# Kernel optimization log

Hardware: AMD Instinct MI355X
Metric: run time of the kernel (lower is better)

Reference implementation:

```python
import jax, jax.numpy as jnp
import numpy as np

HID = 64
HEADS = 4
HEAD_DIM = HID // HEADS
N_MOL, N_PROT = 2048, 4096
E_MOL, E_PROT = 32768, 131072
B = 32


def _lin(key, din, dout):
    kw, kb = jax.random.split(key)
    s = 1.0 / np.sqrt(din)
    W = jax.random.uniform(kw, (din, dout), jnp.float32, -s, s)
    b = jax.random.uniform(kb, (dout,), jnp.float32, -s, s)
    return W, b


def setup_inputs() -> dict:
    key = jax.random.key(0)
    ks = jax.random.split(key, 32)
    inp = {}
    inp['mol_x'] = jax.random.normal(ks[0], (N_MOL, 11), jnp.float32)
    inp['prot_x'] = jax.random.normal(ks[1], (N_PROT, 15), jnp.float32)
    inp['mol_eattr'] = jax.random.normal(ks[2], (E_MOL, 10), jnp.float32)
    inp['prot_eattr'] = jax.random.normal(ks[3], (E_PROT, 10), jnp.float32)
    inp['mol_edge_index'] = jax.random.randint(ks[4], (2, E_MOL), 0, N_MOL, jnp.int32)
    inp['prot_edge_index'] = jax.random.randint(ks[5], (2, E_PROT), 0, N_PROT, jnp.int32)
    inp['mol_batch'] = jnp.sort(jax.random.randint(ks[6], (N_MOL,), 0, B, jnp.int32))
    inp['prot_batch'] = jnp.sort(jax.random.randint(ks[7], (N_PROT,), 0, B, jnp.int32))
    inp['node_lin_mol_W'], inp['node_lin_mol_b'] = _lin(ks[8], 11, HID)
    inp['node_lin_prot_W'], inp['node_lin_prot_b'] = _lin(ks[9], 15, HID)
    inp['edge_lin_mol_W'], inp['edge_lin_mol_b'] = _lin(ks[10], 10, HID)
    inp['edge_lin_prot_W'], inp['edge_lin_prot_b'] = _lin(ks[11], 10, HID)
    for pref, base in (('mol_conv', 12), ('prot_conv', 15)):
        W1s, b1s, W2s, b2s = [], [], [], []
        for l in range(3):
            k1, k2 = jax.random.split(ks[base + l])
            W1, b1 = _lin(k1, HID, HID)
            W2, b2 = _lin(k2, HID, HID)
            W1s.append(W1); b1s.append(b1); W2s.append(W2); b2s.append(b2)
        inp[pref + '_W1'] = jnp.stack(W1s); inp[pref + '_b1'] = jnp.stack(b1s)
        inp[pref + '_W2'] = jnp.stack(W2s); inp[pref + '_b2'] = jnp.stack(b2s)
    for pref, base in (('attn_mp', 18), ('attn_pm', 21)):
        Ws, bs = [], []
        for i in range(3):  # Q, K, V
            W, b = _lin(ks[base + i], HID, HID)
            Ws.append(W); bs.append(b)
        inp[pref + '_W'] = jnp.stack(Ws); inp[pref + '_b'] = jnp.stack(bs)
    inp['fc1_W'], inp['fc1_b'] = _lin(ks[24], 2 * HID, HID)
    inp['fc2_W'], inp['fc2_b'] = _lin(ks[25], HID, 1)
    return inp


def _gine_layer(x, src, dst, eattr, W1, b1, W2, b2):
    # message: ReLU(x_j + e_ji); GINEConv sum aggregation; eps = 0
    msg = jax.nn.relu(x[src] + eattr)                       # [E, H]
    agg = jax.ops.segment_sum(msg, dst, num_segments=x.shape[0])
    h = x + agg
    h = jax.nn.relu(h @ W1 + b1) @ W2 + b2                  # inner MLP
    return jax.nn.relu(h)                                   # post-conv ReLU


def _cross_attn(qn, kn, W, b):
    Nq, Nk = qn.shape[0], kn.shape[0]
    Q = (qn @ W[0] + b[0]).reshape(Nq, HEADS, HEAD_DIM)
    K = (kn @ W[1] + b[1]).reshape(Nk, HEADS, HEAD_DIM)
    V = (kn @ W[2] + b[2]).reshape(Nk, HEADS, HEAD_DIM)
    scores = jnp.einsum('qhd,khd->hqk', Q, K) / np.sqrt(HEAD_DIM)
    w = jax.nn.softmax(scores, axis=-1)
    out = jnp.einsum('hqk,khd->qhd', w, V)
    return out.reshape(Nq, HID)


def _pool(H, batch):
    s = jax.ops.segment_sum(H, batch, num_segments=B)
    c = jax.ops.segment_sum(jnp.ones((H.shape[0],), H.dtype), batch, num_segments=B)
    return s / jnp.maximum(c, 1.0)[:, None]


def _forward(mol_x, prot_x, mol_eattr, prot_eattr,
             node_lin_mol_W, node_lin_mol_b, node_lin_prot_W, node_lin_prot_b,
             edge_lin_mol_W, edge_lin_mol_b, edge_lin_prot_W, edge_lin_prot_b,
             mol_conv_W1, mol_conv_b1, mol_conv_W2, mol_conv_b2,
             prot_conv_W1, prot_conv_b1, prot_conv_W2, prot_conv_b2,
             attn_mp_W, attn_mp_b, attn_pm_W, attn_pm_b,
             fc1_W, fc1_b, fc2_W, fc2_b,
             mol_edge_index, prot_edge_index, mol_batch, prot_batch):
    xm = mol_x @ node_lin_mol_W + node_lin_mol_b
    xp = prot_x @ node_lin_prot_W + node_lin_prot_b
    em = mol_eattr @ edge_lin_mol_W + edge_lin_mol_b
    ep = prot_eattr @ edge_lin_prot_W + edge_lin_prot_b
    ms, md = mol_edge_index[0], mol_edge_index[1]
    ps, pd = prot_edge_index[0], prot_edge_index[1]
    for l in range(3):
        xm = _gine_layer(xm, ms, md, em, mol_conv_W1[l], mol_conv_b1[l], mol_conv_W2[l], mol_conv_b2[l])
    for l in range(3):
        xp = _gine_layer(xp, ps, pd, ep, prot_conv_W1[l], prot_conv_b1[l], prot_conv_W2[l], prot_conv_b2[l])
    H_mol = xm + _cross_attn(xm, xp, attn_mp_W, attn_mp_b)
    H_prot = xp + _cross_attn(xp, xm, attn_pm_W, attn_pm_b)
    z = jnp.concatenate([_pool(H_mol, mol_batch), _pool(H_prot, prot_batch)], axis=1)
    h = jax.nn.relu(z @ fc1_W + fc1_b)
    return jax.nn.sigmoid(h @ fc2_W + fc2_b).squeeze(-1)


def reference(mol_x, prot_x, mol_eattr, prot_eattr,
              node_lin_mol_W, node_lin_mol_b, node_lin_prot_W, node_lin_prot_b,
              edge_lin_mol_W, edge_lin_mol_b, edge_lin_prot_W, edge_lin_prot_b,
              mol_conv_W1, mol_conv_b1, mol_conv_W2, mol_conv_b2,
              prot_conv_W1, prot_conv_b1, prot_conv_W2, prot_conv_b2,
              attn_mp_W, attn_mp_b, attn_pm_W, attn_pm_b,
              fc1_W, fc1_b, fc2_W, fc2_b,
              mol_edge_index, prot_edge_index, mol_batch, prot_batch):
    return _forward(mol_x, prot_x, mol_eattr, prot_eattr,
                    node_lin_mol_W, node_lin_mol_b, node_lin_prot_W, node_lin_prot_b,
                    edge_lin_mol_W, edge_lin_mol_b, edge_lin_prot_W, edge_lin_prot_b,
                    mol_conv_W1, mol_conv_b1, mol_conv_W2, mol_conv_b2,
                    prot_conv_W1, prot_conv_b1, prot_conv_W2, prot_conv_b2,
                    attn_mp_W, attn_mp_b, attn_pm_W, attn_pm_b,
                    fc1_W, fc1_b, fc2_W, fc2_b,
                    mol_edge_index, prot_edge_index, mol_batch, prot_batch)
```

## Files before the change

### kernel.cpp

```cpp
#include <hip/hip_runtime.h>
#include <math.h>

#define HID 64
#define HEADS 4
#define HDIM 16
#define N_MOL 2048
#define N_PROT 4096
#define E_MOL 32768
#define E_PROT 131072
#define BATCH 32
#define N_TOT (N_MOL + N_PROT)
#define E_TOT (E_MOL + E_PROT)
#define CAP 128

#define TQA 16
#define TKA 32
#define KSTA 68
#define CH_MOL 8
#define CH_PROT 2
#define NGRP_MOL (N_MOL / TQA)

#define DOT4(a, b) ((a).x*(b).x + (a).y*(b).y + (a).z*(b).z + (a).w*(b).w)
#define EXP2(x) __builtin_amdgcn_exp2f(x)

__global__ void k_nlb(const float* __restrict__ mol_x, const float* __restrict__ prot_x,
                      const float* __restrict__ Wm, const float* __restrict__ bm,
                      const float* __restrict__ Wp, const float* __restrict__ bp,
                      const int* __restrict__ mol_ei, const int* __restrict__ prot_ei,
                      float* __restrict__ xm, float* __restrict__ xp,
                      int* __restrict__ cursor, int* __restrict__ eidx) {
    if (blockIdx.x < N_TOT / 4) {
        int w = threadIdx.x >> 6, t = threadIdx.x & 63;
        int n = blockIdx.x * 4 + w;
        if (n < N_MOL) {
            const float* xr = mol_x + n * 11;
            float acc = bm[t];
#pragma unroll
            for (int i = 0; i < 11; ++i) acc += xr[i] * Wm[i * HID + t];
            xm[n * HID + t] = acc;
        } else {
            int p = n - N_MOL;
            const float* xr = prot_x + p * 15;
            float acc = bp[t];
#pragma unroll
            for (int i = 0; i < 15; ++i) acc += xr[i] * Wp[i * HID + t];
            xp[p * HID + t] = acc;
        }
    } else {
        int e = (blockIdx.x - N_TOT / 4) * 256 + threadIdx.x;
        int node, loc;
        if (e < E_MOL) { node = mol_ei[E_MOL + e]; loc = e; }
        else { int el = e - E_MOL; node = N_MOL + prot_ei[E_PROT + el]; loc = el; }
        int pos = atomicAdd(&cursor[node], 1);
        eidx[(size_t)node * CAP + pos] = loc;
    }
}

__global__ void k_gine(const float* __restrict__ xin_m, const float* __restrict__ xin_p,
                       float* __restrict__ xout_m, float* __restrict__ xout_p,
                       const float* __restrict__ mol_ea, const float* __restrict__ prot_ea,
                       const int* __restrict__ mol_ei, const int* __restrict__ prot_ei,
                       const float* __restrict__ Wem, const float* __restrict__ bem,
                       const float* __restrict__ Wep, const float* __restrict__ bep,
                       const float* __restrict__ W1m, const float* __restrict__ b1m,
                       const float* __restrict__ W2m, const float* __restrict__ b2m,
                       const float* __restrict__ W1p, const float* __restrict__ b1p,
                       const float* __restrict__ W2p, const float* __restrict__ b2p,
                       const int* __restrict__ cnt, const int* __restrict__ eidx) {
    __shared__ float h0[8][HID];
    __shared__ float h1[8][HID];
    int w = threadIdx.x >> 6, t = threadIdx.x & 63;
    int nb0 = blockIdx.x * 8 + w * 2;
    bool isMol = nb0 < N_MOL;
    const float* x  = isMol ? xin_m : xin_p;
    float* xo       = isMol ? xout_m : xout_p;
    const float* We = isMol ? Wem : Wep;
    float bt        = isMol ? bem[t] : bep[t];
    const float* ea_base = isMol ? mol_ea : prot_ea;
    const int* srcarr    = isMol ? mol_ei : prot_ei;
    int nbias = isMol ? 0 : N_MOL;
    float wcol[10];
#pragma unroll
    for (int i = 0; i < 10; ++i) wcol[i] = We[i * HID + t];

#pragma unroll
    for (int u = 0; u < 2; ++u) {
        int nb = nb0 + u;
        int deg = cnt[nb];
        const int* lst = eidx + (size_t)nb * CAP;
        float agg = 0.f;
        int j = 0;
        for (; j + 1 < deg; j += 2) {
            int e0 = lst[j], e1 = lst[j + 1];
            int s0 = srcarr[e0], s1 = srcarr[e1];
            const float2* p0 = (const float2*)(ea_base + (size_t)e0 * 10);
            const float2* p1 = (const float2*)(ea_base + (size_t)e1 * 10);
            float2 a0 = p0[0], a1 = p0[1], a2 = p0[2], a3 = p0[3], a4 = p0[4];
            float2 c0 = p1[0], c1 = p1[1], c2 = p1[2], c3 = p1[3], c4 = p1[4];
            float xs0 = x[s0 * HID + t];
            float xs1 = x[s1 * HID + t];
            float m0 = bt, m1 = bt;
            m0 = fmaf(a0.x, wcol[0], m0); m0 = fmaf(a0.y, wcol[1], m0);
            m0 = fmaf(a1.x, wcol[2], m0); m0 = fmaf(a1.y, wcol[3], m0);
            m0 = fmaf(a2.x, wcol[4], m0); m0 = fmaf(a2.y, wcol[5], m0);
            m0 = fmaf(a3.x, wcol[6], m0); m0 = fmaf(a3.y, wcol[7], m0);
            m0 = fmaf(a4.x, wcol[8], m0); m0 = fmaf(a4.y, wcol[9], m0);
            m1 = fmaf(c0.x, wcol[0], m1); m1 = fmaf(c0.y, wcol[1], m1);
            m1 = fmaf(c1.x, wcol[2], m1); m1 = fmaf(c1.y, wcol[3], m1);
            m1 = fmaf(c2.x, wcol[4], m1); m1 = fmaf(c2.y, wcol[5], m1);
            m1 = fmaf(c3.x, wcol[6], m1); m1 = fmaf(c3.y, wcol[7], m1);
            m1 = fmaf(c4.x, wcol[8], m1); m1 = fmaf(c4.y, wcol[9], m1);
            agg += fmaxf(m0 + xs0, 0.f) + fmaxf(m1 + xs1, 0.f);
        }
        if (j < deg) {
            int e0 = lst[j];
            int s0 = srcarr[e0];
            const float2* p0 = (const float2*)(ea_base + (size_t)e0 * 10);
            float2 a0 = p0[0], a1 = p0[1], a2 = p0[2], a3 = p0[3], a4 = p0[4];
            float xs0 = x[s0 * HID + t];
            float m0 = bt;
            m0 = fmaf(a0.x, wcol[0], m0); m0 = fmaf(a0.y, wcol[1], m0);
            m0 = fmaf(a1.x, wcol[2], m0); m0 = fmaf(a1.y, wcol[3], m0);
            m0 = fmaf(a2.x, wcol[4], m0); m0 = fmaf(a2.y, wcol[5], m0);
            m0 = fmaf(a3.x, wcol[6], m0); m0 = fmaf(a3.y, wcol[7], m0);
            m0 = fmaf(a4.x, wcol[8], m0); m0 = fmaf(a4.y, wcol[9], m0);
            agg += fmaxf(m0 + xs0, 0.f);
        }
        h0[w * 2 + u][t] = x[(nb0 - nbias + u) * HID + t] + agg;
    }

    const float* W1 = isMol ? W1m : W1p;
    const float* W2 = isMol ? W2m : W2p;
    float b1v = isMol ? b1m[t] : b1p[t];
    float b2v = isMol ? b2m[t] : b2p[t];
    float acc0 = b1v, acc1 = b1v;
    const float4* hA = (const float4*)h0[w * 2];
    const float4* hB = (const float4*)h0[w * 2 + 1];
#pragma unroll
    for (int k = 0; k < 16; ++k) {
        float4 a = hA[k], b = hB[k];
        float w0 = W1[(4 * k + 0) * HID + t], w1 = W1[(4 * k + 1) * HID + t];
        float w2 = W1[(4 * k + 2) * HID + t], w3 = W1[(4 * k + 3) * HID + t];
        acc0 = fmaf(a.x, w0, acc0); acc1 = fmaf(b.x, w0, acc1);
        acc0 = fmaf(a.y, w1, acc0); acc1 = fmaf(b.y, w1, acc1);
        acc0 = fmaf(a.z, w2, acc0); acc1 = fmaf(b.z, w2, acc1);
        acc0 = fmaf(a.w, w3, acc0); acc1 = fmaf(b.w, w3, acc1);
    }
    h1[w * 2][t] = fmaxf(acc0, 0.f);
    h1[w * 2 + 1][t] = fmaxf(acc1, 0.f);
    float d0 = b2v, d1 = b2v;
    const float4* gA = (const float4*)h1[w * 2];
    const float4* gB = (const float4*)h1[w * 2 + 1];
#pragma unroll
    for (int k = 0; k < 16; ++k) {
        float4 a = gA[k], b = gB[k];
        float w0 = W2[(4 * k + 0) * HID + t], w1 = W2[(4 * k + 1) * HID + t];
        float w2 = W2[(4 * k + 2) * HID + t], w3 = W2[(4 * k + 3) * HID + t];
        d0 = fmaf(a.x, w0, d0); d1 = fmaf(b.x, w0, d1);
        d0 = fmaf(a.y, w1, d0); d1 = fmaf(b.y, w1, d1);
        d0 = fmaf(a.z, w2, d0); d1 = fmaf(b.z, w2, d1);
        d0 = fmaf(a.w, w3, d0); d1 = fmaf(b.w, w3, d1);
    }
    int n0 = nb0 - nbias;
    xo[n0 * HID + t] = fmaxf(d0, 0.f);
    xo[(n0 + 1) * HID + t] = fmaxf(d1, 0.f);
}

__global__ void k_qkv(const float* __restrict__ xm, const float* __restrict__ xp,
                      const float* __restrict__ mpW, const float* __restrict__ mpb,
                      const float* __restrict__ pmW, const float* __restrict__ pmb,
                      float* __restrict__ Qm, float* __restrict__ Kp, float* __restrict__ Vp,
                      float* __restrict__ Qp, float* __restrict__ Km, float* __restrict__ Vm) {
    __shared__ float row[8][HID];
    int w = threadIdx.x >> 6, t = threadIdx.x & 63;
    int b0 = blockIdx.x * 8;
    const float *src, *W, *bias;
    float* dst;
    int base;
    if (b0 < 2048)       { base = 0;     src = xm; W = mpW;        bias = mpb;       dst = Qm; }
    else if (b0 < 6144)  { base = 2048;  src = xp; W = mpW + 4096; bias = mpb + 64;  dst = Kp; }
    else if (b0 < 10240) { base = 6144;  src = xp; W = mpW + 8192; bias = mpb + 128; dst = Vp; }
    else if (b0 < 14336) { base = 10240; src = xp; W = pmW;        bias = pmb;       dst = Qp; }
    else if (b0 < 16384) { base = 14336; src = xm; W = pmW + 4096; bias = pmb + 64;  dst = Km; }
    else                 { base = 16384; src = xm; W = pmW + 8192; bias = pmb + 128; dst = Vm; }
    int n0 = b0 - base + w * 2, n1 = n0 + 1;
    row[w * 2][t] = src[n0 * HID + t];
    row[w * 2 + 1][t] = src[n1 * HID + t];
    float acc0 = bias[t], acc1 = acc0;
    const float4* rA = (const float4*)row[w * 2];
    const float4* rB = (const float4*)row[w * 2 + 1];
#pragma unroll
    for (int k = 0; k < 16; ++k) {
        float4 a = rA[k], b = rB[k];
        float w0 = W[(4 * k + 0) * HID + t], w1 = W[(4 * k + 1) * HID + t];
        float w2 = W[(4 * k + 2) * HID + t], w3 = W[(4 * k + 3) * HID + t];
        acc0 = fmaf(a.x, w0, acc0); acc1 = fmaf(b.x, w0, acc1);
        acc0 = fmaf(a.y, w1, acc0); acc1 = fmaf(b.y, w1, acc1);
        acc0 = fmaf(a.z, w2, acc0); acc1 = fmaf(b.z, w2, acc1);
        acc0 = fmaf(a.w, w3, acc0); acc1 = fmaf(b.w, w3, acc1);
    }
    dst[n0 * HID + t] = acc0;
    dst[n1 * HID + t] = acc1;
}

__device__ inline void upd4(float4& A, const float4 v0, const float4 v1,
                            float p0, float p1, float al) {
    A.x = fmaf(p1, v1.x, fmaf(p0, v0.x, A.x * al));
    A.y = fmaf(p1, v1.y, fmaf(p0, v0.y, A.y * al));
    A.z = fmaf(p1, v1.z, fmaf(p0, v0.z, A.z * al));
    A.w = fmaf(p1, v1.w, fmaf(p0, v0.w, A.w * al));
}

__device__ inline void merge4(float4& A, const float4 B, float c1, float c2) {
    A.x = A.x * c1 + B.x * c2;
    A.y = A.y * c1 + B.y * c2;
    A.z = A.z * c1 + B.z * c2;
    A.w = A.w * c1 + B.w * c2;
}

__device__ inline float4 shfl4(const float4 a, int off) {
    float4 r;
    r.x = __shfl_xor(a.x, off, 64); r.y = __shfl_xor(a.y, off, 64);
    r.z = __shfl_xor(a.z, off, 64); r.w = __shfl_xor(a.w, off, 64);
    return r;
}

__global__ __launch_bounds__(256) void k_attn(
    const float* __restrict__ Qm, const float* __restrict__ Kp, const float* __restrict__ Vp,
    const float* __restrict__ Qp, const float* __restrict__ Km, const float* __restrict__ Vm,
    float* __restrict__ part_m, float* __restrict__ part_p) {
    __shared__ float Kl[2][TKA * KSTA];
    __shared__ float Vl[2][TKA * KSTA];

    int t = threadIdx.x;
    const float *Q, *K, *V;
    float* part;
    int q0, chunk, CH, KC;
    {
        int b = blockIdx.x;
        const int MOLB = NGRP_MOL * CH_MOL;
        if (b < MOLB) {
            chunk = b & 7; q0 = (b >> 3) * TQA; CH = CH_MOL; KC = N_PROT / CH_MOL;
            Q = Qm; K = Kp; V = Vp; part = part_m;
        } else {
            b -= MOLB;
            chunk = b & 1; q0 = (b >> 1) * TQA; CH = CH_PROT; KC = N_MOL / CH_PROT;
            Q = Qp; K = Km; V = Vm; part = part_p;
        }
    }
    int kbeg = chunk * KC;

    int sub = t & 15, h = (t >> 4) & 3, qg = t >> 6;
    int r0 = t >> 4;
    int c0 = (t & 15) << 2;

    const float sc = 0.25f * 1.44269504088896f;
    float4 q4[4][4];
#pragma unroll
    for (int qq = 0; qq < 4; ++qq) {
        const float4* Qr = (const float4*)(Q + (q0 + qg * 4 + qq) * HID + h * HDIM);
#pragma unroll
        for (int j = 0; j < 4; ++j) {
            float4 v = Qr[j];
            v.x *= sc; v.y *= sc; v.z *= sc; v.w *= sc;
            q4[qq][j] = v;
        }
    }

    float mreg[4], lreg[4];
    float4 A[4][4];
#pragma unroll
    for (int qq = 0; qq < 4; ++qq) {
        mreg[qq] = -INFINITY; lreg[qq] = 0.f;
#pragma unroll
        for (int j = 0; j < 4; ++j) A[qq][j] = (float4){0.f, 0.f, 0.f, 0.f};
    }

    {
        const float4* Kg = (const float4*)(K + kbeg * HID);
        const float4* Vg = (const float4*)(V + kbeg * HID);
        float4 ka = Kg[t], kb = Kg[t + 256];
        float4 va = Vg[t], vb = Vg[t + 256];
        *(float4*)&Kl[0][r0 * KSTA + c0] = ka;
        *(float4*)&Kl[0][(r0 + 16) * KSTA + c0] = kb;
        *(float4*)&Vl[0][r0 * KSTA + c0] = va;
        *(float4*)&Vl[0][(r0 + 16) * KSTA + c0] = vb;
    }
    __syncthreads();

    const int NT = KC / TKA;
    for (int tile = 0; tile < NT; ++tile) {
        int cur = tile & 1;
        float4 ka, kb, va, vb;
        bool more = (tile + 1) < NT;
        if (more) {
            const float4* Kg = (const float4*)(K + (kbeg + (tile + 1) * TKA) * HID);
            const float4* Vg = (const float4*)(V + (kbeg + (tile + 1) * TKA) * HID);
            ka = Kg[t]; kb = Kg[t + 256];
            va = Vg[t]; vb = Vg[t + 256];
        }

        const float4* Kr0 = (const float4*)&Kl[cur][sub * KSTA + h * HDIM];
        const float4* Kr1 = (const float4*)&Kl[cur][(sub + 16) * KSTA + h * HDIM];
        float4 x0 = Kr0[0], x1 = Kr0[1], x2 = Kr0[2], x3 = Kr0[3];
        float4 y0 = Kr1[0], y1 = Kr1[1], y2 = Kr1[2], y3 = Kr1[3];

        float s0[4], s1[4];
#pragma unroll
        for (int qq = 0; qq < 4; ++qq) {
            s0[qq] = DOT4(x0, q4[qq][0]) + DOT4(x1, q4[qq][1]) + DOT4(x2, q4[qq][2]) + DOT4(x3, q4[qq][3]);
            s1[qq] = DOT4(y0, q4[qq][0]) + DOT4(y1, q4[qq][1]) + DOT4(y2, q4[qq][2]) + DOT4(y3, q4[qq][3]);
        }

        const float4* Vr0 = (const float4*)&Vl[cur][sub * KSTA + h * HDIM];
        const float4* Vr1 = (const float4*)&Vl[cur][(sub + 16) * KSTA + h * HDIM];
        float4 v00 = Vr0[0], v01 = Vr0[1], v02 = Vr0[2], v03 = Vr0[3];
        float4 v10 = Vr1[0], v11 = Vr1[1], v12 = Vr1[2], v13 = Vr1[3];

#pragma unroll
        for (int qq = 0; qq < 4; ++qq) {
            float mn = fmaxf(mreg[qq], fmaxf(s0[qq], s1[qq]));
            float al = EXP2(mreg[qq] - mn);
            float p0 = EXP2(s0[qq] - mn);
            float p1 = EXP2(s1[qq] - mn);
            lreg[qq] = lreg[qq] * al + p0 + p1;
            upd4(A[qq][0], v00, v10, p0, p1, al);
            upd4(A[qq][1], v01, v11, p0, p1, al);
            upd4(A[qq][2], v02, v12, p0, p1, al);
            upd4(A[qq][3], v03, v13, p0, p1, al);
            mreg[qq] = mn;
        }

        if (more) {
            int nxt = cur ^ 1;
            *(float4*)&Kl[nxt][r0 * KSTA + c0] = ka;
            *(float4*)&Kl[nxt][(r0 + 16) * KSTA + c0] = kb;
            *(float4*)&Vl[nxt][r0 * KSTA + c0] = va;
            *(float4*)&Vl[nxt][(r0 + 16) * KSTA + c0] = vb;
        }
        __syncthreads();
    }

#pragma unroll
    for (int off = 1; off < 16; off <<= 1) {
#pragma unroll
        for (int qq = 0; qq < 4; ++qq) {
            float m2 = __shfl_xor(mreg[qq], off, 64);
            float l2 = __shfl_xor(lreg[qq], off, 64);
            float4 B0 = shfl4(A[qq][0], off), B1 = shfl4(A[qq][1], off);
            float4 B2 = shfl4(A[qq][2], off), B3 = shfl4(A[qq][3], off);
            float mn = fmaxf(mreg[qq], m2);
            float c1 = EXP2(mreg[qq] - mn), c2 = EXP2(m2 - mn);
            lreg[qq] = lreg[qq] * c1 + l2 * c2;
            merge4(A[qq][0], B0, c1, c2); merge4(A[qq][1], B1, c1, c2);
            merge4(A[qq][2], B2, c1, c2); merge4(A[qq][3], B3, c1, c2);
            mreg[qq] = mn;
        }
    }

    if (sub == 0) {
#pragma unroll
        for (int qq = 0; qq < 4; ++qq) {
            int qi = q0 + qg * 4 + qq;
            float* pp = part + (size_t)((qi * HEADS + h) * CH + chunk) * 20;
            pp[0] = mreg[qq]; pp[1] = lreg[qq];
            *(float4*)&pp[4] = A[qq][0]; *(float4*)&pp[8] = A[qq][1];
            *(float4*)&pp[12] = A[qq][2]; *(float4*)&pp[16] = A[qq][3];
        }
    }
}

__global__ void k_final(const float* __restrict__ part_m, const float* __restrict__ part_p,
                        const float* __restrict__ xm, const float* __restrict__ xp,
                        const int* __restrict__ mb, const int* __restrict__ pb,
                        const float* __restrict__ fc1W, const float* __restrict__ fc1b,
                        const float* __restrict__ fc2W, const float* __restrict__ fc2b,
                        float* __restrict__ out) {
    __shared__ float sm[64][65];
    __shared__ float z[2 * HID];
    int b = blockIdx.x;
    int t = threadIdx.x;
    int h = t & 3, s = t >> 2;
    int ms, me, ps, pe;
    {
        int lo = 0, hi = N_MOL;
        while (lo < hi) { int mid = (lo + hi) >> 1; if (mb[mid] < b) lo = mid + 1; else hi = mid; }
        ms = lo; lo = ms; hi = N_MOL;
        while (lo < hi) { int mid = (lo + hi) >> 1; if (mb[mid] < b + 1) lo = mid + 1; else hi = mid; }
        me = lo;
        lo = 0; hi = N_PROT;
        while (lo < hi) { int mid = (lo + hi) >> 1; if (pb[mid] < b) lo = mid + 1; else hi = mid; }
        ps = lo; lo = ps; hi = N_PROT;
        while (lo < hi) { int mid = (lo + hi) >> 1; if (pb[mid] < b + 1) lo = mid + 1; else hi = mid; }
        pe = lo;
    }

    {
        float acc[16];
#pragma unroll
        for (int d = 0; d < 16; ++d) acc[d] = 0.f;
        for (int q = ms + s; q < me; q += 64) {
            const float* p0 = part_m + (size_t)(q * HEADS + h) * CH_MOL * 20;
            float mmax = -INFINITY;
#pragma unroll
            for (int c = 0; c < CH_MOL; ++c) mmax = fmaxf(mmax, p0[c * 20]);
            float lsum = 0.f, wgt[CH_MOL];
#pragma unroll
            for (int c = 0; c < CH_MOL; ++c) {
                wgt[c] = EXP2(p0[c * 20] - mmax);
                lsum += p0[c * 20 + 1] * wgt[c];
            }
            float inv = 1.f / lsum;
            const float* Xr = xm + q * HID + h * HDIM;
#pragma unroll
            for (int d = 0; d < 16; ++d) {
                float o = Xr[d];
#pragma unroll
                for (int c = 0; c < CH_MOL; ++c)
                    o = fmaf(p0[c * 20 + 4 + d], wgt[c] * inv, o);
                acc[d] += o;
            }
        }
#pragma unroll
        for (int d = 0; d < 16; ++d) sm[s][h * 16 + d] = acc[d];
    }
    __syncthreads();
    if (t < 64) {
        float sum = 0.f;
        for (int ss = 0; ss < 64; ++ss) sum += sm[ss][t];
        z[t] = sum / fmaxf((float)(me - ms), 1.f);
    }
    __syncthreads();

    {
        float acc[16];
#pragma unroll
        for (int d = 0; d < 16; ++d) acc[d] = 0.f;
        for (int q = ps + s; q < pe; q += 64) {
            const float* p0 = part_p + (size_t)(q * HEADS + h) * CH_PROT * 20;
            float m0 = p0[0], m1 = p0[20];
            float mmax = fmaxf(m0, m1);
            float w0 = EXP2(m0 - mmax), w1 = EXP2(m1 - mmax);
            float inv = 1.f / (p0[1] * w0 + p0[21] * w1);
            w0 *= inv; w1 *= inv;
            const float* Xr = xp + q * HID + h * HDIM;
#pragma unroll
            for (int d = 0; d < 16; ++d)
                acc[d] += Xr[d] + p0[4 + d] * w0 + p0[24 + d] * w1;
        }
#pragma unroll
        for (int d = 0; d < 16; ++d) sm[s][h * 16 + d] = acc[d];
    }
    __syncthreads();
    if (t < 64) {
        float sum = 0.f;
        for (int ss = 0; ss < 64; ++ss) sum += sm[ss][t];
        z[64 + t] = sum / fmaxf((float)(pe - ps), 1.f);
    }
    __syncthreads();

    if (t < 64) {
        float acc = fc1b[t];
        const float4* zv = (const float4*)z;
#pragma unroll
        for (int k = 0; k < 32; ++k) {
            float4 hv = zv[k];
            acc = fmaf(hv.x, fc1W[(4 * k + 0) * 64 + t], acc);
            acc = fmaf(hv.y, fc1W[(4 * k + 1) * 64 + t], acc);
            acc = fmaf(hv.z, fc1W[(4 * k + 2) * 64 + t], acc);
            acc = fmaf(hv.w, fc1W[(4 * k + 3) * 64 + t], acc);
        }
        float hv = fmaxf(acc, 0.f);
        float prod = hv * fc2W[t];
#pragma unroll
        for (int off = 32; off > 0; off >>= 1) prod += __shfl_xor(prod, off, 64);
        if (t == 0) out[b] = 1.f / (1.f + __expf(-(prod + fc2b[0])));
    }
}

extern "C" void kernel_launch(void* const* d_in, const int* in_sizes, int n_in,
                              void* d_out, int out_size, void* d_ws, size_t ws_size,
                              hipStream_t stream) {
    const float* mol_x   = (const float*)d_in[0];
    const float* prot_x  = (const float*)d_in[1];
    const float* mol_ea  = (const float*)d_in[2];
    const float* prot_ea = (const float*)d_in[3];
    const int*   mol_ei  = (const int*)d_in[4];
    const int*   prot_ei = (const int*)d_in[5];
    const int*   mol_b   = (const int*)d_in[6];
    const int*   prot_b  = (const int*)d_in[7];
    const float* nlmW = (const float*)d_in[8];
    const float* nlmb = (const float*)d_in[9];
    const float* nlpW = (const float*)d_in[10];
    const float* nlpb = (const float*)d_in[11];
    const float* elmW = (const float*)d_in[12];
    const float* elmb = (const float*)d_in[13];
    const float* elpW = (const float*)d_in[14];
    const float* elpb = (const float*)d_in[15];
    const float* mcW1 = (const float*)d_in[16];
    const float* mcb1 = (const float*)d_in[17];
    const float* mcW2 = (const float*)d_in[18];
    const float* mcb2 = (const float*)d_in[19];
    const float* pcW1 = (const float*)d_in[20];
    const float* pcb1 = (const float*)d_in[21];
    const float* pcW2 = (const float*)d_in[22];
    const float* pcb2 = (const float*)d_in[23];
    const float* mpW  = (const float*)d_in[24];
    const float* mpb  = (const float*)d_in[25];
    const float* pmW  = (const float*)d_in[26];
    const float* pmb  = (const float*)d_in[27];
    const float* fc1W = (const float*)d_in[28];
    const float* fc1b = (const float*)d_in[29];
    const float* fc2W = (const float*)d_in[30];
    const float* fc2b = (const float*)d_in[31];

    float* ws    = (float*)d_ws;
    float* xa_m  = ws;
    float* xa_p  = xa_m + 131072;
    float* xb_m  = xa_p + 262144;
    float* xb_p  = xb_m + 131072;
    float* Qm    = xb_p + 262144;
    float* Kp    = Qm + 131072;
    float* Vp    = Kp + 262144;
    float* Qp    = Vp + 262144;
    float* Km    = Qp + 262144;
    float* Vm    = Km + 131072;
    float* partm = Vm + 131072;
    float* partp = partm + 1310720;
    int* cursor  = (int*)(partp + 655360);
    int* eidx    = (int*)partm;

    hipMemsetAsync(cursor, 0, (size_t)N_TOT * 4, stream);

    k_nlb<<<N_TOT / 4 + E_TOT / 256, 256, 0, stream>>>(
        mol_x, prot_x, nlmW, nlmb, nlpW, nlpb, mol_ei, prot_ei, xa_m, xa_p, cursor, eidx);

    k_gine<<<N_TOT / 8, 256, 0, stream>>>(xa_m, xa_p, xb_m, xb_p, mol_ea, prot_ea, mol_ei, prot_ei,
        elmW, elmb, elpW, elpb,
        mcW1, mcb1, mcW2, mcb2, pcW1, pcb1, pcW2, pcb2, cursor, eidx);
    k_gine<<<N_TOT / 8, 256, 0, stream>>>(xb_m, xb_p, xa_m, xa_p, mol_ea, prot_ea, mol_ei, prot_ei,
        elmW, elmb, elpW, elpb,
        mcW1 + 4096, mcb1 + 64, mcW2 + 4096, mcb2 + 64,
        pcW1 + 4096, pcb1 + 64, pcW2 + 4096, pcb2 + 64, cursor, eidx);
    k_gine<<<N_TOT / 8, 256, 0, stream>>>(xa_m, xa_p, xb_m, xb_p, mol_ea, prot_ea, mol_ei, prot_ei,
        elmW, elmb, elpW, elpb,
        mcW1 + 8192, mcb1 + 128, mcW2 + 8192, mcb2 + 128,
        pcW1 + 8192, pcb1 + 128, pcW2 + 8192, pcb2 + 128, cursor, eidx);

    k_qkv<<<18432 / 8, 256, 0, stream>>>(xb_m, xb_p, mpW, mpb, pmW, pmb, Qm, Kp, Vp, Qp, Km, Vm);
    k_attn<<<NGRP_MOL * CH_MOL + (N_PROT / TQA) * CH_PROT, 256, 0, stream>>>(
        Qm, Kp, Vp, Qp, Km, Vm, partm, partp);

    k_final<<<BATCH, 256, 0, stream>>>(partm, partp, xb_m, xb_p, mol_b, prot_b,
                                       fc1W, fc1b, fc2W, fc2b, (float*)d_out);
}
```

Before: 385.4 us.

## Fuse all stages into one cooperative persistent kernel with grid syncs

Replaces the memset and seven separate kernel launches with a single cooperative kernel. Blocks loop over virtual block indices for each stage: edge bucketing, the three GINE layers, QKV, attention and the final pooling, with grid-wide syncs in between. The mol attention key split drops from 8 to 4 chunks so fewer partials need storing and merging. This removes launch gaps and inter-kernel drain, but it caps the grid at 1024 blocks, adds grid barrier costs, and the union shared memory sized for attention may limit occupancy.

After: 1.406 ms. +264.9%, slower.

```diff
diff --git a/kernel.cpp b/kernel.cpp
--- a/kernel.cpp
+++ b/kernel.cpp
@@ -1,4 +1,5 @@
 #include <hip/hip_runtime.h>
+#include <hip/hip_cooperative_groups.h>
 #include <math.h>
 
 #define HID 64
@@ -16,68 +17,68 @@
 #define TQA 16
 #define TKA 32
 #define KSTA 68
-#define CH_MOL 8
+#define CH_MOL 4
 #define CH_PROT 2
+#define KCHUNK 1024
 #define NGRP_MOL (N_MOL / TQA)
+#define ATTN_VB (NGRP_MOL * CH_MOL + (N_PROT / TQA) * CH_PROT)
 
 #define DOT4(a, b) ((a).x*(b).x + (a).y*(b).y + (a).z*(b).z + (a).w*(b).w)
 #define EXP2(x) __builtin_amdgcn_exp2f(x)
 
-__global__ void k_nlb(const float* __restrict__ mol_x, const float* __restrict__ prot_x,
-                      const float* __restrict__ Wm, const float* __restrict__ bm,
-                      const float* __restrict__ Wp, const float* __restrict__ bp,
-                      const int* __restrict__ mol_ei, const int* __restrict__ prot_ei,
-                      float* __restrict__ xm, float* __restrict__ xp,
-                      int* __restrict__ cursor, int* __restrict__ eidx) {
-    if (blockIdx.x < N_TOT / 4) {
-        int w = threadIdx.x >> 6, t = threadIdx.x & 63;
-        int n = blockIdx.x * 4 + w;
-        if (n < N_MOL) {
-            const float* xr = mol_x + n * 11;
-            float acc = bm[t];
-#pragma unroll
-            for (int i = 0; i < 11; ++i) acc += xr[i] * Wm[i * HID + t];
-            xm[n * HID + t] = acc;
-        } else {
-            int p = n - N_MOL;
-            const float* xr = prot_x + p * 15;
-            float acc = bp[t];
-#pragma unroll
-            for (int i = 0; i < 15; ++i) acc += xr[i] * Wp[i * HID + t];
-            xp[p * HID + t] = acc;
-        }
-    } else {
-        int e = (blockIdx.x - N_TOT / 4) * 256 + threadIdx.x;
-        int node, loc;
-        if (e < E_MOL) { node = mol_ei[E_MOL + e]; loc = e; }
-        else { int el = e - E_MOL; node = N_MOL + prot_ei[E_PROT + el]; loc = el; }
-        int pos = atomicAdd(&cursor[node], 1);
-        eidx[(size_t)node * CAP + pos] = loc;
-    }
+struct Prm {
+    const float *mol_x, *prot_x, *mol_ea, *prot_ea;
+    const int *mol_ei, *prot_ei, *mol_b, *prot_b;
+    const float *nlmW, *nlmb, *nlpW, *nlpb, *elmW, *elmb, *elpW, *elpb;
+    const float *mcW1, *mcb1, *mcW2, *mcb2, *pcW1, *pcb1, *pcW2, *pcb2;
+    const float *mpW, *mpb, *pmW, *pmb, *fc1W, *fc1b, *fc2W, *fc2b;
+    float *xa_m, *xa_p, *xb_m, *xb_p, *Qm, *Kp, *Vp, *Qp, *Km, *Vm, *partm, *partp;
+    int *cursor, *eidx;
+    float* out;
+};
+
+union SMem {
+    struct { float Kl[2][TKA * KSTA]; float Vl[2][TKA * KSTA]; } attn;
+    struct { float h0[8][HID]; float h1[8][HID]; } gine;
+    struct { float row[8][HID]; } qkv;
+    struct { float red[64][65]; float z[2 * HID]; } fin;
+};
+
+__device__ inline void upd4(float4& A, const float4 v0, const float4 v1,
+                            float p0, float p1, float al) {
+    A.x = fmaf(p1, v1.x, fmaf(p0, v0.x, A.x * al));
+    A.y = fmaf(p1, v1.y, fmaf(p0, v0.y, A.y * al));
+    A.z = fmaf(p1, v1.z, fmaf(p0, v0.z, A.z * al));
+    A.w = fmaf(p1, v1.w, fmaf(p0, v0.w, A.w * al));
 }
-
-__global__ void k_gine(const float* __restrict__ xin_m, const float* __restrict__ xin_p,
-                       float* __restrict__ xout_m, float* __restrict__ xout_p,
-                       const float* __restrict__ mol_ea, const float* __restrict__ prot_ea,
-                       const int* __restrict__ mol_ei, const int* __restrict__ prot_ei,
-                       const float* __restrict__ Wem, const float* __restrict__ bem,
-                       const float* __restrict__ Wep, const float* __restrict__ bep,
-                       const float* __restrict__ W1m, const float* __restrict__ b1m,
-                       const float* __restrict__ W2m, const float* __restrict__ b2m,
-                       const float* __restrict__ W1p, const float* __restrict__ b1p,
-                       const float* __restrict__ W2p, const float* __restrict__ b2p,
-                       const int* __restrict__ cnt, const int* __restrict__ eidx) {
-    __shared__ float h0[8][HID];
-    __shared__ float h1[8][HID];
+__device__ inline void merge4(float4& A, const float4 B, float c1, float c2) {
+    A.x = A.x * c1 + B.x * c2;
+    A.y = A.y * c1 + B.y * c2;
+    A.z = A.z * c1 + B.z * c2;
+    A.w = A.w * c1 + B.w * c2;
+}
+__device__ inline float4 shfl4(const float4 a, int off) {
+    float4 r;
+    r.x = __shfl_xor(a.x, off, 64); r.y = __shfl_xor(a.y, off, 64);
+    r.z = __shfl_xor(a.z, off, 64); r.w = __shfl_xor(a.w, off, 64);
+    return r;
+}
+
+__device__ __forceinline__ void gine_layer(
+    int vb, const float* xin_m, const float* xin_p, float* xout_m, float* xout_p,
+    const Prm& p, const float* Wem, const float* bem, const float* Wep, const float* bep,
+    const float* W1m, const float* b1m, const float* W2m, const float* b2m,
+    const float* W1p, const float* b1p, const float* W2p, const float* b2p,
+    float (*h0)[HID], float (*h1)[HID]) {
     int w = threadIdx.x >> 6, t = threadIdx.x & 63;
-    int nb0 = blockIdx.x * 8 + w * 2;
+    int nb0 = vb * 8 + w * 2;
     bool isMol = nb0 < N_MOL;
     const float* x  = isMol ? xin_m : xin_p;
     float* xo       = isMol ? xout_m : xout_p;
     const float* We = isMol ? Wem : Wep;
     float bt        = isMol ? bem[t] : bep[t];
-    const float* ea_base = isMol ? mol_ea : prot_ea;
-    const int* srcarr    = isMol ? mol_ei : prot_ei;
+    const float* ea_base = isMol ? p.mol_ea : p.prot_ea;
+    const int* srcarr    = isMol ? p.mol_ei : p.prot_ei;
     int nbias = isMol ? 0 : N_MOL;
     float wcol[10];
 #pragma unroll
@@ -85,18 +86,18 @@
 
 #pragma unroll
     for (int u = 0; u < 2; ++u) {
-        int nb = nb0 + u;
-        int deg = cnt[nb];
-        const int* lst = eidx + (size_t)nb * CAP;
+        int nbx = nb0 + u;
+        int deg = p.cursor[nbx];
+        const int* lst = p.eidx + (size_t)nbx * CAP;
         float agg = 0.f;
         int j = 0;
         for (; j + 1 < deg; j += 2) {
             int e0 = lst[j], e1 = lst[j + 1];
             int s0 = srcarr[e0], s1 = srcarr[e1];
-            const float2* p0 = (const float2*)(ea_base + (size_t)e0 * 10);
-            const float2* p1 = (const float2*)(ea_base + (size_t)e1 * 10);
-            float2 a0 = p0[0], a1 = p0[1], a2 = p0[2], a3 = p0[3], a4 = p0[4];
-            float2 c0 = p1[0], c1 = p1[1], c2 = p1[2], c3 = p1[3], c4 = p1[4];
+            const float2* q0 = (const float2*)(ea_base + (size_t)e0 * 10);
+            const float2* q1 = (const float2*)(ea_base + (size_t)e1 * 10);
+            float2 a0 = q0[0], a1 = q0[1], a2 = q0[2], a3 = q0[3], a4 = q0[4];
+            float2 c0 = q1[0], c1 = q1[1], c2 = q1[2], c3 = q1[3], c4 = q1[4];
             float xs0 = x[s0 * HID + t];
             float xs1 = x[s1 * HID + t];
             float m0 = bt, m1 = bt;
@@ -115,8 +116,8 @@
         if (j < deg) {
             int e0 = lst[j];
             int s0 = srcarr[e0];
-            const float2* p0 = (const float2*)(ea_base + (size_t)e0 * 10);
-            float2 a0 = p0[0], a1 = p0[1], a2 = p0[2], a3 = p0[3], a4 = p0[4];
+            const float2* q0 = (const float2*)(ea_base + (size_t)e0 * 10);
+            float2 a0 = q0[0], a1 = q0[1], a2 = q0[2], a3 = q0[3], a4 = q0[4];
             float xs0 = x[s0 * HID + t];
             float m0 = bt;
             m0 = fmaf(a0.x, wcol[0], m0); m0 = fmaf(a0.y, wcol[1], m0);
@@ -166,391 +167,396 @@
     xo[(n0 + 1) * HID + t] = fmaxf(d1, 0.f);
 }
 
-__global__ void k_qkv(const float* __restrict__ xm, const float* __restrict__ xp,
-                      const float* __restrict__ mpW, const float* __restrict__ mpb,
-                      const float* __restrict__ pmW, const float* __restrict__ pmb,
-                      float* __restrict__ Qm, float* __restrict__ Kp, float* __restrict__ Vp,
-                      float* __restrict__ Qp, float* __restrict__ Km, float* __restrict__ Vm) {
-    __shared__ float row[8][HID];
-    int w = threadIdx.x >> 6, t = threadIdx.x & 63;
-    int b0 = blockIdx.x * 8;
-    const float *src, *W, *bias;
-    float* dst;
-    int base;
-    if (b0 < 2048)       { base = 0;     src = xm; W = mpW;        bias = mpb;       dst = Qm; }
-    else if (b0 < 6144)  { base = 2048;  src = xp; W = mpW + 4096; bias = mpb + 64;  dst = Kp; }
-    else if (b0 < 10240) { base = 6144;  src = xp; W = mpW + 8192; bias = mpb + 128; dst = Vp; }
-    else if (b0 < 14336) { base = 10240; src = xp; W = pmW;        bias = pmb;       dst = Qp; }
-    else if (b0 < 16384) { base = 14336; src = xm; W = pmW + 4096; bias = pmb + 64;  dst = Km; }
-    else                 { base = 16384; src = xm; W = pmW + 8192; bias = pmb + 128; dst = Vm; }
-    int n0 = b0 - base + w * 2, n1 = n0 + 1;
-    row[w * 2][t] = src[n0 * HID + t];
-    row[w * 2 + 1][t] = src[n1 * HID + t];
-    float acc0 = bias[t], acc1 = acc0;
-    const float4* rA = (const float4*)row[w * 2];
-    const float4* rB = (const float4*)row[w * 2 + 1];
-#pragma unroll
-    for (int k = 0; k < 16; ++k) {
-        float4 a = rA[k], b = rB[k];
-        float w0 = W[(4 * k + 0) * HID + t], w1 = W[(4 * k + 1) * HID + t];
-        float w2 = W[(4 * k + 2) * HID + t], w3 = W[(4 * k + 3) * HID + t];
-        acc0 = fmaf(a.x, w0, acc0); acc1 = fmaf(b.x, w0, acc1);
-        acc0 = fmaf(a.y, w1, acc0); acc1 = fmaf(b.y, w1, acc1);
-        acc0 = fmaf(a.z, w2, acc0); acc1 = fmaf(b.z, w2, acc1);
-        acc0 = fmaf(a.w, w3, acc0); acc1 = fmaf(b.w, w3, acc1);
-    }
-    dst[n0 * HID + t] = acc0;
-    dst[n1 * HID + t] = acc1;
-}
-
-__device__ inline void upd4(float4& A, const float4 v0, const float4 v1,
-                            float p0, float p1, float al) {
-    A.x = fmaf(p1, v1.x, fmaf(p0, v0.x, A.x * al));
-    A.y = fmaf(p1, v1.y, fmaf(p0, v0.y, A.y * al));
-    A.z = fmaf(p1, v1.z, fmaf(p0, v0.z, A.z * al));
-    A.w = fmaf(p1, v1.w, fmaf(p0, v0.w, A.w * al));
-}
-
-__device__ inline void merge4(float4& A, const float4 B, float c1, float c2) {
-    A.x = A.x * c1 + B.x * c2;
-    A.y = A.y * c1 + B.y * c2;
-    A.z = A.z * c1 + B.z * c2;
-    A.w = A.w * c1 + B.w * c2;
-}
-
-__device__ inline float4 shfl4(const float4 a, int off) {
-    float4 r;
-    r.x = __shfl_xor(a.x, off, 64); r.y = __shfl_xor(a.y, off, 64);
-    r.z = __shfl_xor(a.z, off, 64); r.w = __shfl_xor(a.w, off, 64);
-    return r;
-}
-
-__global__ __launch_bounds__(256) void k_attn(
-    const float* __restrict__ Qm, const float* __restrict__ Kp, const float* __restrict__ Vp,
-    const float* __restrict__ Qp, const float* __restrict__ Km, const float* __restrict__ Vm,
-    float* __restrict__ part_m, float* __restrict__ part_p) {
-    __shared__ float Kl[2][TKA * KSTA];
-    __shared__ float Vl[2][TKA * KSTA];
-
-    int t = threadIdx.x;
-    const float *Q, *K, *V;
-    float* part;
-    int q0, chunk, CH, KC;
-    {
-        int b = blockIdx.x;
-        const int MOLB = NGRP_MOL * CH_MOL;
-        if (b < MOLB) {
-            chunk = b & 7; q0 = (b >> 3) * TQA; CH = CH_MOL; KC = N_PROT / CH_MOL;
-            Q = Qm; K = Kp; V = Vp; part = part_m;
+__global__ __launch_bounds__(256, 4) void k_mega(Prm p) {
+    cooperative_groups::grid_group gg = cooperative_groups::this_grid();
+    __shared__ SMem smem;
+    const int t = threadIdx.x;
+    const int nb = gridDim.x;
+
+    for (int i = blockIdx.x * 256 + t; i < N_TOT; i += nb * 256) p.cursor[i] = 0;
+    gg.sync();
+
+    for (int vb = blockIdx.x; vb < N_TOT / 4 + E_TOT / 256; vb += nb) {
+        if (vb < N_TOT / 4) {
+            int w = t >> 6, l = t & 63;
+            int n = vb * 4 + w;
+            if (n < N_MOL) {
+                const float* xr = p.mol_x + n * 11;
+                float acc = p.nlmb[l];
+#pragma unroll
+                for (int i = 0; i < 11; ++i) acc += xr[i] * p.nlmW[i * HID + l];
+                p.xa_m[n * HID + l] = acc;
+            } else {
+                int q = n - N_MOL;
+                const float* xr = p.prot_x + q * 15;
+                float acc = p.nlpb[l];
+#pragma unroll
+                for (int i = 0; i < 15; ++i) acc += xr[i] * p.nlpW[i * HID + l];
+                p.xa_p[q * HID + l] = acc;
+            }
         } else {
-            b -= MOLB;
-            chunk = b & 1; q0 = (b >> 1) * TQA; CH = CH_PROT; KC = N_MOL / CH_PROT;
-            Q = Qp; K = Km; V = Vm; part = part_p;
-        }
-    }
-    int kbeg = chunk * KC;
-
-    int sub = t & 15, h = (t >> 4) & 3, qg = t >> 6;
-    int r0 = t >> 4;
-    int c0 = (t & 15) << 2;
-
-    const float sc = 0.25f * 1.44269504088896f;
-    float4 q4[4][4];
-#pragma unroll
-    for (int qq = 0; qq < 4; ++qq) {
-        const float4* Qr = (const float4*)(Q + (q0 + qg * 4 + qq) * HID + h * HDIM);
-#pragma unroll
-        for (int j = 0; j < 4; ++j) {
-            float4 v = Qr[j];
-            v.x *= sc; v.y *= sc; v.z *= sc; v.w *= sc;
-            q4[qq][j] = v;
-        }
-    }
-
-    float mreg[4], lreg[4];
-    float4 A[4][4];
-#pragma unroll
-    for (int qq = 0; qq < 4; ++qq) {
-        mreg[qq] = -INFINITY; lreg[qq] = 0.f;
-#pragma unroll
-        for (int j = 0; j < 4; ++j) A[qq][j] = (float4){0.f, 0.f, 0.f, 0.f};
-    }
-
-    {
-        const float4* Kg = (const float4*)(K + kbeg * HID);
-        const float4* Vg = (const float4*)(V + kbeg * HID);
-        float4 ka = Kg[t], kb = Kg[t + 256];
-        float4 va = Vg[t], vb = Vg[t + 256];
-        *(float4*)&Kl[0][r0 * KSTA + c0] = ka;
-        *(float4*)&Kl[0][(r0 + 16) * KSTA + c0] = kb;
-        *(float4*)&Vl[0][r0 * KSTA + c0] = va;
-        *(float4*)&Vl[0][(r0 + 16) * KSTA + c0] = vb;
-    }
-    __syncthreads();
-
-    const int NT = KC / TKA;
-    for (int tile = 0; tile < NT; ++tile) {
-        int cur = tile & 1;
-        float4 ka, kb, va, vb;
-        bool more = (tile + 1) < NT;
-        if (more) {
-            const float4* Kg = (const float4*)(K + (kbeg + (tile + 1) * TKA) * HID);
-            const float4* Vg = (const float4*)(V + (kbeg + (tile + 1) * TKA) * HID);
-            ka = Kg[t]; kb = Kg[t + 256];
-            va = Vg[t]; vb = Vg[t + 256];
-        }
-
-        const float4* Kr0 = (const float4*)&Kl[cur][sub * KSTA + h * HDIM];
-        const float4* Kr1 = (const float4*)&Kl[cur][(sub + 16) * KSTA + h * HDIM];
-        float4 x0 = Kr0[0], x1 = Kr0[1], x2 = Kr0[2], x3 = Kr0[3];
-        float4 y0 = Kr1[0], y1 = Kr1[1], y2 = Kr1[2], y3 = Kr1[3];
-
-        float s0[4], s1[4];
+            int e = (vb - N_TOT / 4) * 256 + t;
+            int node, loc;
+            if (e < E_MOL) { node = p.mol_ei[E_MOL + e]; loc = e; }
+            else { int el = e - E_MOL; node = N_MOL + p.prot_ei[E_PROT + el]; loc = el; }
+            int pos = atomicAdd(&p.cursor[node], 1);
+            p.eidx[(size_t)node * CAP + pos] = loc;
+        }
+    }
+    gg.sync();
+
+    for (int vb = blockIdx.x; vb < N_TOT / 8; vb += nb)
+        gine_layer(vb, p.xa_m, p.xa_p, p.xb_m, p.xb_p, p,
+                   p.elmW, p.elmb, p.elpW, p.elpb,
+                   p.mcW1, p.mcb1, p.mcW2, p.mcb2,
+                   p.pcW1, p.pcb1, p.pcW2, p.pcb2, smem.gine.h0, smem.gine.h1);
+    gg.sync();
+    for (int vb = blockIdx.x; vb < N_TOT / 8; vb += nb)
+        gine_layer(vb, p.xb_m, p.xb_p, p.xa_m, p.xa_p, p,
+                   p.elmW, p.elmb, p.elpW, p.elpb,
+                   p.mcW1 + 4096, p.mcb1 + 64, p.mcW2 + 4096, p.mcb2 + 64,
+                   p.pcW1 + 4096, p.pcb1 + 64, p.pcW2 + 4096, p.pcb2 + 64,
+                   smem.gine.h0, smem.gine.h1);
+    gg.sync();
+    for (int vb = blockIdx.x; vb < N_TOT / 8; vb += nb)
+        gine_layer(vb, p.xa_m, p.xa_p, p.xb_m, p.xb_p, p,
+                   p.elmW, p.elmb, p.elpW, p.elpb,
+                   p.mcW1 + 8192, p.mcb1 + 128, p.mcW2 + 8192, p.mcb2 + 128,
+                   p.pcW1 + 8192, p.pcb1 + 128, p.pcW2 + 8192, p.pcb2 + 128,
+                   smem.gine.h0, smem.gine.h1);
+    gg.sync();
+
+    for (int vb = blockIdx.x; vb < 18432 / 8; vb += nb) {
+        int w = t >> 6, l = t & 63;
+        int b0 = vb * 8;
+        const float *src, *W, *bias;
+        float* dst;
+        int base;
+        if (b0 < 2048)       { base = 0;     src = p.xb_m; W = p.mpW;        bias = p.mpb;       dst = p.Qm; }
+        else if (b0 < 6144)  { base = 2048;  src = p.xb_p; W = p.mpW + 4096; bias = p.mpb + 64;  dst = p.Kp; }
+        else if (b0 < 10240) { base = 6144;  src = p.xb_p; W = p.mpW + 8192; bias = p.mpb + 128; dst = p.Vp; }
+        else if (b0 < 14336) { base = 10240; src = p.xb_p; W = p.pmW;        bias = p.pmb;       dst = p.Qp; }
+        else if (b0 < 16384) { base = 14336; src = p.xb_m; W = p.pmW + 4096; bias = p.pmb + 64;  dst = p.Km; }
+        else                 { base = 16384; src = p.xb_m; W = p.pmW + 8192; bias = p.pmb + 128; dst = p.Vm; }
+        int n0 = b0 - base + w * 2, n1 = n0 + 1;
+        smem.qkv.row[w * 2][l] = src[n0 * HID + l];
+        smem.qkv.row[w * 2 + 1][l] = src[n1 * HID + l];
+        float acc0 = bias[l], acc1 = acc0;
+        const float4* rA = (const float4*)smem.qkv.row[w * 2];
+        const float4* rB = (const float4*)smem.qkv.row[w * 2 + 1];
+#pragma unroll
+        for (int k = 0; k < 16; ++k) {
+            float4 a = rA[k], b = rB[k];
+            float w0 = W[(4 * k + 0) * HID + l], w1 = W[(4 * k + 1) * HID + l];
+            float w2 = W[(4 * k + 2) * HID + l], w3 = W[(4 * k + 3) * HID + l];
+            acc0 = fmaf(a.x, w0, acc0); acc1 = fmaf(b.x, w0, acc1);
+            acc0 = fmaf(a.y, w1, acc0); acc1 = fmaf(b.y, w1, acc1);
+            acc0 = fmaf(a.z, w2, acc0); acc1 = fmaf(b.z, w2, acc1);
+            acc0 = fmaf(a.w, w3, acc0); acc1 = fmaf(b.w, w3, acc1);
+        }
+        dst[n0 * HID + l] = acc0;
+        dst[n1 * HID + l] = acc1;
+    }
+    gg.sync();
+
+    for (int vb0 = blockIdx.x; vb0 < ATTN_VB; vb0 += nb) {
+        const float *Q, *K, *V;
+        float* part;
+        int q0, chunk, CH;
+        {
+            int b = vb0;
+            const int MOLB = NGRP_MOL * CH_MOL;
+            if (b < MOLB) {
+                chunk = b & 3; q0 = (b >> 2) * TQA; CH = CH_MOL;
+                Q = p.Qm; K = p.Kp; V = p.Vp; part = p.partm;
+            } else {
+                b -= MOLB;
+                chunk = b & 1; q0 = (b >> 1) * TQA; CH = CH_PROT;
+                Q = p.Qp; K = p.Km; V = p.Vm; part = p.partp;
+            }
+        }
+        int kbeg = chunk * KCHUNK;
+
+        int sub = t & 15, h = (t >> 4) & 3, qg = t >> 6;
+        int r0 = t >> 4, c0 = (t & 15) << 2;
+
+        const float sc = 0.25f * 1.44269504088896f;
+        float4 q4[4][4];
 #pragma unroll
         for (int qq = 0; qq < 4; ++qq) {
-            s0[qq] = DOT4(x0, q4[qq][0]) + DOT4(x1, q4[qq][1]) + DOT4(x2, q4[qq][2]) + DOT4(x3, q4[qq][3]);
-            s1[qq] = DOT4(y0, q4[qq][0]) + DOT4(y1, q4[qq][1]) + DOT4(y2, q4[qq][2]) + DOT4(y3, q4[qq][3]);
-        }
-
-        const float4* Vr0 = (const float4*)&Vl[cur][sub * KSTA + h * HDIM];
-        const float4* Vr1 = (const float4*)&Vl[cur][(sub + 16) * KSTA + h * HDIM];
-        float4 v00 = Vr0[0], v01 = Vr0[1], v02 = Vr0[2], v03 = Vr0[3];
-        float4 v10 = Vr1[0], v11 = Vr1[1], v12 = Vr1[2], v13 = Vr1[3];
-
+            const float4* Qr = (const float4*)(Q + (q0 + qg * 4 + qq) * HID + h * HDIM);
+#pragma unroll
+            for (int j = 0; j < 4; ++j) {
+                float4 v = Qr[j];
+                v.x *= sc; v.y *= sc; v.z *= sc; v.w *= sc;
+                q4[qq][j] = v;
+            }
+        }
+
+        float mreg[4], lreg[4];
+        float4 A[4][4];
 #pragma unroll
         for (int qq = 0; qq < 4; ++qq) {
-            float mn = fmaxf(mreg[qq], fmaxf(s0[qq], s1[qq]));
-            float al = EXP2(mreg[qq] - mn);
-            float p0 = EXP2(s0[qq] - mn);
-            float p1 = EXP2(s1[qq] - mn);
-            lreg[qq] = lreg[qq] * al + p0 + p1;
-            upd4(A[qq][0], v00, v10, p0, p1, al);
-            upd4(A[qq][1], v01, v11, p0, p1, al);
-            upd4(A[qq][2], v02, v12, p0, p1, al);
-            upd4(A[qq][3], v03, v13, p0, p1, al);
-            mreg[qq] = mn;
-        }
-
-        if (more) {
-            int nxt = cur ^ 1;
-            *(float4*)&Kl[nxt][r0 * KSTA + c0] = ka;
-            *(float4*)&Kl[nxt][(r0 + 16) * KSTA + c0] = kb;
-            *(float4*)&Vl[nxt][r0 * KSTA + c0] = va;
-            *(float4*)&Vl[nxt][(r0 + 16) * KSTA + c0] = vb;
-        }
-        __syncthreads();
-    }
-
-#pragma unroll
-    for (int off = 1; off < 16; off <<= 1) {
-#pragma unroll
-        for (int qq = 0; qq < 4; ++qq) {
-            float m2 = __shfl_xor(mreg[qq], off, 64);
-            float l2 = __shfl_xor(lreg[qq], off, 64);
-            float4 B0 = shfl4(A[qq][0], off), B1 = shfl4(A[qq][1], off);
-            float4 B2 = shfl4(A[qq][2], off), B3 = shfl4(A[qq][3], off);
-            float mn = fmaxf(mreg[qq], m2);
-            float c1 = EXP2(mreg[qq] - mn), c2 = EXP2(m2 - mn);
-            lreg[qq] = lreg[qq] * c1 + l2 * c2;
-            merge4(A[qq][0], B0, c1, c2); merge4(A[qq][1], B1, c1, c2);
-            merge4(A[qq][2], B2, c1, c2); merge4(A[qq][3], B3, c1, c2);
-            mreg[qq] = mn;
-        }
-    }
-
-    if (sub == 0) {
-#pragma unroll
-        for (int qq = 0; qq < 4; ++qq) {
-            int qi = q0 + qg * 4 + qq;
-            float* pp = part + (size_t)((qi * HEADS + h) * CH + chunk) * 20;
-            pp[0] = mreg[qq]; pp[1] = lreg[qq];
-            *(float4*)&pp[4] = A[qq][0]; *(float4*)&pp[8] = A[qq][1];
-            *(float4*)&pp[12] = A[qq][2]; *(float4*)&pp[16] = A[qq][3];
-        }
-    }
-}
-
-__global__ void k_final(const float* __restrict__ part_m, const float* __restrict__ part_p,
-                        const float* __restrict__ xm, const float* __restrict__ xp,
-                        const int* __restrict__ mb, const int* __restrict__ pb,
-                        const float* __restrict__ fc1W, const float* __restrict__ fc1b,
-                        const float* __restrict__ fc2W, const float* __restrict__ fc2b,
-                        float* __restrict__ out) {
-    __shared__ float sm[64][65];
-    __shared__ float z[2 * HID];
-    int b = blockIdx.x;
-    int t = threadIdx.x;
-    int h = t & 3, s = t >> 2;
-    int ms, me, ps, pe;
-    {
-        int lo = 0, hi = N_MOL;
-        while (lo < hi) { int mid = (lo + hi) >> 1; if (mb[mid] < b) lo = mid + 1; else hi = mid; }
-        ms = lo; lo = ms; hi = N_MOL;
-        while (lo < hi) { int mid = (lo + hi) >> 1; if (mb[mid] < b + 1) lo = mid + 1; else hi = mid; }
-        me = lo;
-        lo = 0; hi = N_PROT;
-        while (lo < hi) { int mid = (lo + hi) >> 1; if (pb[mid] < b) lo = mid + 1; else hi = mid; }
-        ps = lo; lo = ps; hi = N_PROT;
-        while (lo < hi) { int mid = (lo + hi) >> 1; if (pb[mid] < b + 1) lo = mid + 1; else hi = mid; }
-        pe = lo;
-    }
-
-    {
-        float acc[16];
-#pragma unroll
-        for (int d = 0; d < 16; ++d) acc[d] = 0.f;
-        for (int q = ms + s; q < me; q += 64) {
-            const float* p0 = part_m + (size_t)(q * HEADS + h) * CH_MOL * 20;
-            float mmax = -INFINITY;
-#pragma unroll
-            for (int c = 0; c < CH_MOL; ++c) mmax = fmaxf(mmax, p0[c * 20]);
-            float lsum = 0.f, wgt[CH_MOL];
-#pragma unroll
-            for (int c = 0; c < CH_MOL; ++c) {
-                wgt[c] = EXP2(p0[c * 20] - mmax);
-                lsum += p0[c * 20 + 1] * wgt[c];
-            }
-            float inv = 1.f / lsum;
-            const float* Xr = xm + q * HID + h * HDIM;
-#pragma unroll
-            for (int d = 0; d < 16; ++d) {
-                float o = Xr[d];
-#pragma unroll
-                for (int c = 0; c < CH_MOL; ++c)
-                    o = fmaf(p0[c * 20 + 4 + d], wgt[c] * inv, o);
-                acc[d] += o;
-            }
-        }
-#pragma unroll
-        for (int d = 0; d < 16; ++d) sm[s][h * 16 + d] = acc[d];
-    }
-    __syncthreads();
-    if (t < 64) {
-        float sum = 0.f;
-        for (int ss = 0; ss < 64; ++ss) sum += sm[ss][t];
-        z[t] = sum / fmaxf((float)(me - ms), 1.f);
-    }
-    __syncthreads();
-
-    {
-        float acc[16];
-#pragma unroll
-        for (int d = 0; d < 16; ++d) acc[d] = 0.f;
-        for (int q = ps + s; q < pe; q += 64) {
-            const float* p0 = part_p + (size_t)(q * HEADS + h) * CH_PROT * 20;
-            float m0 = p0[0], m1 = p0[20];
-            float mmax = fmaxf(m0, m1);
-            float w0 = EXP2(m0 - mmax), w1 = EXP2(m1 - mmax);
-            float inv = 1.f / (p0[1] * w0 + p0[21] * w1);
-            w0 *= inv; w1 *= inv;
-            const float* Xr = xp + q * HID + h * HDIM;
-#pragma unroll
-            for (int d = 0; d < 16; ++d)
-                acc[d] += Xr[d] + p0[4 + d] * w0 + p0[24 + d] * w1;
-        }
-#pragma unroll
-        for (int d = 0; d < 16; ++d) sm[s][h * 16 + d] = acc[d];
-    }
-    __syncthreads();
-    if (t < 64) {
-        float sum = 0.f;
-        for (int ss = 0; ss < 64; ++ss) sum += sm[ss][t];
-        z[64 + t] = sum / fmaxf((float)(pe - ps), 1.f);
-    }
-    __syncthreads();
-
-    if (t < 64) {
-        float acc = fc1b[t];
-        const float4* zv = (const float4*)z;
-#pragma unroll
-        for (int k = 0; k < 32; ++k) {
-            float4 hv = zv[k];
-            acc = fmaf(hv.x, fc1W[(4 * k + 0) * 64 + t], acc);
-            acc = fmaf(hv.y, fc1W[(4 * k + 1) * 64 + t], acc);
-            acc = fmaf(hv.z, fc1W[(4 * k + 2) * 64 + t], acc);
-            acc = fmaf(hv.w, fc1W[(4 * k + 3) * 64 + t], acc);
-        }
-        float hv = fmaxf(acc, 0.f);
-        float prod = hv * fc2W[t];
-#pragma unroll
-        for (int off = 32; off > 0; off >>= 1) prod += __shfl_xor(prod, off, 64);
-        if (t == 0) out[b] = 1.f / (1.f + __expf(-(prod + fc2b[0])));
+            mreg[qq] = -INFINITY; lreg[qq] = 0.f;
+#pragma unroll
+            for (int j = 0; j < 4; ++j) A[qq][j] = (float4){0.f, 0.f, 0.f, 0.f};
+        }
+
+        __syncthreads();
+        {
+            const float4* Kg = (const float4*)(K + kbeg * HID);
+            const float4* Vg = (const float4*)(V + kbeg * HID);
+            float4 ka = Kg[t], kb = Kg[t + 256];
+            float4 va = Vg[t], vb = Vg[t + 256];
+            *(float4*)&smem.attn.Kl[0][r0 * KSTA + c0] = ka;
+            *(float4*)&smem.attn.Kl[0][(r0 + 16) * KSTA + c0] = kb;
+            *(float4*)&smem.attn.Vl[0][r0 * KSTA + c0] = va;
+            *(float4*)&smem.attn.Vl[0][(r0 + 16) * KSTA + c0] = vb;
+        }
+        __syncthreads();
+
+        const int NT = KCHUNK / TKA;
+        for (int tile = 0; tile < NT; ++tile) {
+            int cur = tile & 1;
+            float4 ka, kb, va, vv;
+            bool more = (tile + 1) < NT;
+            if (more) {
+                const float4* Kg = (const float4*)(K + (kbeg + (tile + 1) * TKA) * HID);
+                const float4* Vg = (const float4*)(V + (kbeg + (tile + 1) * TKA) * HID);
+                ka = Kg[t]; kb = Kg[t + 256];
+                va = Vg[t]; vv = Vg[t + 256];
+            }
+
+            const float4* Kr0 = (const float4*)&smem.attn.Kl[cur][sub * KSTA + h * HDIM];
+            const float4* Kr1 = (const float4*)&smem.attn.Kl[cur][(sub + 16) * KSTA + h * HDIM];
+            float4 x0 = Kr0[0], x1 = Kr0[1], x2 = Kr0[2], x3 = Kr0[3];
+            float4 y0 = Kr1[0], y1 = Kr1[1], y2 = Kr1[2], y3 = Kr1[3];
+
+            float s0[4], s1[4];
+#pragma unroll
+            for (int qq = 0; qq < 4; ++qq) {
+                s0[qq] = DOT4(x0, q4[qq][0]) + DOT4(x1, q4[qq][1]) + DOT4(x2, q4[qq][2]) + DOT4(x3, q4[qq][3]);
+                s1[qq] = DOT4(y0, q4[qq][0]) + DOT4(y1, q4[qq][1]) + DOT4(y2, q4[qq][2]) + DOT4(y3, q4[qq][3]);
+            }
+
+            const float4* Vr0 = (const float4*)&smem.attn.Vl[cur][sub * KSTA + h * HDIM];
+            const float4* Vr1 = (const float4*)&smem.attn.Vl[cur][(sub + 16) * KSTA + h * HDIM];
+            float4 v00 = Vr0[0], v01 = Vr0[1], v02 = Vr0[2], v03 = Vr0[3];
+            float4 v10 = Vr1[0], v11 = Vr1[1], v12 = Vr1[2], v13 = Vr1[3];
+
+#pragma unroll
+            for (int qq = 0; qq < 4; ++qq) {
+                float mn = fmaxf(mreg[qq], fmaxf(s0[qq], s1[qq]));
+                float al = EXP2(mreg[qq] - mn);
+                float p0 = EXP2(s0[qq] - mn);
+                float p1 = EXP2(s1[qq] - mn);
+                lreg[qq] = lreg[qq] * al + p0 + p1;
+                upd4(A[qq][0], v00, v10, p0, p1, al);
+                upd4(A[qq][1], v01, v11, p0, p1, al);
+                upd4(A[qq][2], v02, v12, p0, p1, al);
+                upd4(A[qq][3], v03, v13, p0, p1, al);
+                mreg[qq] = mn;
+            }
+
+            if (more) {
+                int nxt = cur ^ 1;
+                *(float4*)&smem.attn.Kl[nxt][r0 * KSTA + c0] = ka;
+                *(float4*)&smem.attn.Kl[nxt][(r0 + 16) * KSTA + c0] = kb;
+                *(float4*)&smem.attn.Vl[nxt][r0 * KSTA + c0] = va;
+                *(float4*)&smem.attn.Vl[nxt][(r0 + 16) * KSTA + c0] = vv;
+            }
+            __syncthreads();
+        }
+
+#pragma unroll
+        for (int off = 1; off < 16; off <<= 1) {
+#pragma unroll
+            for (int qq = 0; qq < 4; ++qq) {
+                float m2 = __shfl_xor(mreg[qq], off, 64);
+                float l2 = __shfl_xor(lreg[qq], off, 64);
+                float4 B0 = shfl4(A[qq][0], off), B1 = shfl4(A[qq][1], off);
+                float4 B2 = shfl4(A[qq][2], off), B3 = shfl4(A[qq][3], off);
+                float mn = fmaxf(mreg[qq], m2);
+                float c1 = EXP2(mreg[qq] - mn), c2 = EXP2(m2 - mn);
+                lreg[qq] = lreg[qq] * c1 + l2 * c2;
+                merge4(A[qq][0], B0, c1, c2); merge4(A[qq][1], B1, c1, c2);
+                merge4(A[qq][2], B2, c1, c2); merge4(A[qq][3], B3, c1, c2);
+                mreg[qq] = mn;
+            }
+        }
+
+        if (sub == 0) {
+#pragma unroll
+            for (int qq = 0; qq < 4; ++qq) {
+                int qi = q0 + qg * 4 + qq;
+                float* pp = part + (size_t)((qi * HEADS + h) * CH + chunk) * 20;
+                pp[0] = mreg[qq]; pp[1] = lreg[qq];
+                *(float4*)&pp[4] = A[qq][0]; *(float4*)&pp[8] = A[qq][1];
+                *(float4*)&pp[12] = A[qq][2]; *(float4*)&pp[16] = A[qq][3];
+            }
+        }
+    }
+    gg.sync();
+
+    for (int b = blockIdx.x; b < BATCH; b += nb) {
+        int h = t & 3, s = t >> 2;
+        int ms, me, ps, pe;
+        {
+            int lo = 0, hi = N_MOL;
+            while (lo < hi) { int mid = (lo + hi) >> 1; if (p.mol_b[mid] < b) lo = mid + 1; else hi = mid; }
+            ms = lo; lo = ms; hi = N_MOL;
+            while (lo < hi) { int mid = (lo + hi) >> 1; if (p.mol_b[mid] < b + 1) lo = mid + 1; else hi = mid; }
+            me = lo;
+            lo = 0; hi = N_PROT;
+            while (lo < hi) { int mid = (lo + hi) >> 1; if (p.prot_b[mid] < b) lo = mid + 1; else hi = mid; }
+            ps = lo; lo = ps; hi = N_PROT;
+            while (lo < hi) { int mid = (lo + hi) >> 1; if (p.prot_b[mid] < b + 1) lo = mid + 1; else hi = mid; }
+            pe = lo;
+        }
+        __syncthreads();
+        {
+            float acc[16];
+#pragma unroll
+            for (int d = 0; d < 16; ++d) acc[d] = 0.f;
+            for (int q = ms + s; q < me; q += 64) {
+                const float* p0 = p.partm + (size_t)(q * HEADS + h) * CH_MOL * 20;
+                float mmax = -INFINITY;
+#pragma unroll
+                for (int c = 0; c < CH_MOL; ++c) mmax = fmaxf(mmax, p0[c * 20]);
+                float lsum = 0.f, wgt[CH_MOL];
+#pragma unroll
+                for (int c = 0; c < CH_MOL; ++c) {
+                    wgt[c] = EXP2(p0[c * 20] - mmax);
+                    lsum += p0[c * 20 + 1] * wgt[c];
+                }
+                float inv = 1.f / lsum;
+                const float* Xr = p.xb_m + q * HID + h * HDIM;
+#pragma unroll
+                for (int d = 0; d < 16; ++d) {
+                    float o = Xr[d];
+#pragma unroll
+                    for (int c = 0; c < CH_MOL; ++c)
+                        o = fmaf(p0[c * 20 + 4 + d], wgt[c] * inv, o);
+                    acc[d] += o;
+                }
+            }
+#pragma unroll
+            for (int d = 0; d < 16; ++d) smem.fin.red[s][h * 16 + d] = acc[d];
+        }
+        __syncthreads();
+        if (t < 64) {
+            float sum = 0.f;
+            for (int ss = 0; ss < 64; ++ss) sum += smem.fin.red[ss][t];
+            smem.fin.z[t] = sum / fmaxf((float)(me - ms), 1.f);
+        }
+        __syncthreads();
+        {
+            float acc[16];
+#pragma unroll
+            for (int d = 0; d < 16; ++d) acc[d] = 0.f;
+            for (int q = ps + s; q < pe; q += 64) {
+                const float* p0 = p.partp + (size_t)(q * HEADS + h) * CH_PROT * 20;
+                float m0 = p0[0], m1 = p0[20];
+                float mmax = fmaxf(m0, m1);
+                float w0 = EXP2(m0 - mmax), w1 = EXP2(m1 - mmax);
+                float inv = 1.f / (p0[1] * w0 + p0[21] * w1);
+                w0 *= inv; w1 *= inv;
+                const float* Xr = p.xb_p + q * HID + h * HDIM;
+#pragma unroll
+                for (int d = 0; d < 16; ++d)
+                    acc[d] += Xr[d] + p0[4 + d] * w0 + p0[24 + d] * w1;
+            }
+#pragma unroll
+            for (int d = 0; d < 16; ++d) smem.fin.red[s][h * 16 + d] = acc[d];
+        }
+        __syncthreads();
+        if (t < 64) {
+            float sum = 0.f;
+            for (int ss = 0; ss < 64; ++ss) sum += smem.fin.red[ss][t];
+            smem.fin.z[64 + t] = sum / fmaxf((float)(pe - ps), 1.f);
+        }
+        __syncthreads();
+        if (t < 64) {
+            float acc = p.fc1b[t];
+            const float4* zv = (const float4*)smem.fin.z;
+#pragma unroll
+            for (int k = 0; k < 32; ++k) {
+                float4 hv = zv[k];
+                acc = fmaf(hv.x, p.fc1W[(4 * k + 0) * 64 + t], acc);
+                acc = fmaf(hv.y, p.fc1W[(4 * k + 1) * 64 + t], acc);
+                acc = fmaf(hv.z, p.fc1W[(4 * k + 2) * 64 + t], acc);
+                acc = fmaf(hv.w, p.fc1W[(4 * k + 3) * 64 + t], acc);
+            }
+            float hv = fmaxf(acc, 0.f);
+            float prod = hv * p.fc2W[t];
+#pragma unroll
+            for (int off = 32; off > 0; off >>= 1) prod += __shfl_xor(prod, off, 64);
+            if (t == 0) p.out[b] = 1.f / (1.f + __expf(-(prod + p.fc2b[0])));
+        }
+        __syncthreads();
     }
 }
 
 extern "C" void kernel_launch(void* const* d_in, const int* in_sizes, int n_in,
                               void* d_out, int out_size, void* d_ws, size_t ws_size,
                               hipStream_t stream) {
-    const float* mol_x   = (const float*)d_in[0];
-    const float* prot_x  = (const float*)d_in[1];
-    const float* mol_ea  = (const float*)d_in[2];
-    const float* prot_ea = (const float*)d_in[3];
-    const int*   mol_ei  = (const int*)d_in[4];
-    const int*   prot_ei = (const int*)d_in[5];
-    const int*   mol_b   = (const int*)d_in[6];
-    const int*   prot_b  = (const int*)d_in[7];
-    const float* nlmW = (const float*)d_in[8];
-    const float* nlmb = (const float*)d_in[9];
-    const float* nlpW = (const float*)d_in[10];
-    const float* nlpb = (const float*)d_in[11];
-    const float* elmW = (const float*)d_in[12];
-    const float* elmb = (const float*)d_in[13];
-    const float* elpW = (const float*)d_in[14];
-    const float* elpb = (const float*)d_in[15];
-    const float* mcW1 = (const float*)d_in[16];
-    const float* mcb1 = (const float*)d_in[17];
-    const float* mcW2 = (const float*)d_in[18];
-    const float* mcb2 = (const float*)d_in[19];
-    const float* pcW1 = (const float*)d_in[20];
-    const float* pcb1 = (const float*)d_in[21];
-    const float* pcW2 = (const float*)d_in[22];
-    const float* pcb2 = (const float*)d_in[23];
-    const float* mpW  = (const float*)d_in[24];
-    const float* mpb  = (const float*)d_in[25];
-    const float* pmW  = (const float*)d_in[26];
-    const float* pmb  = (const float*)d_in[27];
-    const float* fc1W = (const float*)d_in[28];
-    const float* fc1b = (const float*)d_in[29];
-    const float* fc2W = (const float*)d_in[30];
-    const float* fc2b = (const float*)d_in[31];
-
-    float* ws    = (float*)d_ws;
-    float* xa_m  = ws;
-    float* xa_p  = xa_m + 131072;
-    float* xb_m  = xa_p + 262144;
-    float* xb_p  = xb_m + 131072;
-    float* Qm    = xb_p + 262144;
-    float* Kp    = Qm + 131072;
-    float* Vp    = Kp + 262144;
-    float* Qp    = Vp + 262144;
-    float* Km    = Qp + 262144;
-    float* Vm    = Km + 131072;
-    float* partm = Vm + 131072;
-    float* partp = partm + 1310720;
-    int* cursor  = (int*)(partp + 655360);
-    int* eidx    = (int*)partm;
-
-    hipMemsetAsync(cursor, 0, (size_t)N_TOT * 4, stream);
-
-    k_nlb<<<N_TOT / 4 + E_TOT / 256, 256, 0, stream>>>(
-        mol_x, prot_x, nlmW, nlmb, nlpW, nlpb, mol_ei, prot_ei, xa_m, xa_p, cursor, eidx);
-
-    k_gine<<<N_TOT / 8, 256, 0, stream>>>(xa_m, xa_p, xb_m, xb_p, mol_ea, prot_ea, mol_ei, prot_ei,
-        elmW, elmb, elpW, elpb,
-        mcW1, mcb1, mcW2, mcb2, pcW1, pcb1, pcW2, pcb2, cursor, eidx);
-    k_gine<<<N_TOT / 8, 256, 0, stream>>>(xb_m, xb_p, xa_m, xa_p, mol_ea, prot_ea, mol_ei, prot_ei,
-        elmW, elmb, elpW, elpb,
-        mcW1 + 4096, mcb1 + 64, mcW2 + 4096, mcb2 + 64,
-        pcW1 + 4096, pcb1 + 64, pcW2 + 4096, pcb2 + 64, cursor, eidx);
-    k_gine<<<N_TOT / 8, 256, 0, stream>>>(xa_m, xa_p, xb_m, xb_p, mol_ea, prot_ea, mol_ei, prot_ei,
-        elmW, elmb, elpW, elpb,
-        mcW1 + 8192, mcb1 + 128, mcW2 + 8192, mcb2 + 128,
-        pcW1 + 8192, pcb1 + 128, pcW2 + 8192, pcb2 + 128, cursor, eidx);
-
-    k_qkv<<<18432 / 8, 256, 0, stream>>>(xb_m, xb_p, mpW, mpb, pmW, pmb, Qm, Kp, Vp, Qp, Km, Vm);
-    k_attn<<<NGRP_MOL * CH_MOL + (N_PROT / TQA) * CH_PROT, 256, 0, stream>>>(
-        Qm, Kp, Vp, Qp, Km, Vm, partm, partp);
-
-    k_final<<<BATCH, 256, 0, stream>>>(partm, partp, xb_m, xb_p, mol_b, prot_b,
-                                       fc1W, fc1b, fc2W, fc2b, (float*)d_out);
+    Prm p;
+    p.mol_x   = (const float*)d_in[0];
+    p.prot_x  = (const float*)d_in[1];
+    p.mol_ea  = (const float*)d_in[2];
+    p.prot_ea = (const float*)d_in[3];
+    p.mol_ei  = (const int*)d_in[4];
+    p.prot_ei = (const int*)d_in[5];
+    p.mol_b   = (const int*)d_in[6];
+    p.prot_b  = (const int*)d_in[7];
+    p.nlmW = (const float*)d_in[8];
+    p.nlmb = (const float*)d_in[9];
+    p.nlpW = (const float*)d_in[10];
+    p.nlpb = (const float*)d_in[11];
+    p.elmW = (const float*)d_in[12];
+    p.elmb = (const float*)d_in[13];
+    p.elpW = (const float*)d_in[14];
+    p.elpb = (const float*)d_in[15];
+    p.mcW1 = (const float*)d_in[16];
+    p.mcb1 = (const float*)d_in[17];
+    p.mcW2 = (const float*)d_in[18];
+    p.mcb2 = (const float*)d_in[19];
+    p.pcW1 = (const float*)d_in[20];
+    p.pcb1 = (const float*)d_in[21];
+    p.pcW2 = (const float*)d_in[22];
+    p.pcb2 = (const float*)d_in[23];
+    p.mpW  = (const float*)d_in[24];
+    p.mpb  = (const float*)d_in[25];
+    p.pmW  = (const float*)d_in[26];
+    p.pmb  = (const float*)d_in[27];
+    p.fc1W = (const float*)d_in[28];
+    p.fc1b = (const float*)d_in[29];
+    p.fc2W = (const float*)d_in[30];
+    p.fc2b = (const float*)d_in[31];
+
+    float* ws = (float*)d_ws;
+    p.xa_m  = ws;
+    p.xa_p  = p.xa_m + 131072;
+    p.xb_m  = p.xa_p + 262144;
+    p.xb_p  = p.xb_m + 131072;
+    p.Qm    = p.xb_p + 262144;
+    p.Kp    = p.Qm + 131072;
+    p.Vp    = p.Kp + 262144;
+    p.Qp    = p.Vp + 262144;
+    p.Km    = p.Qp + 262144;
+    p.Vm    = p.Km + 131072;
+    p.partm = p.Vm + 131072;
+    p.partp = p.partm + 655360;
+    p.cursor = (int*)(p.partp + 655360);
+    p.eidx  = (int*)p.partm;
+    p.out   = (float*)d_out;
+
+    int blocksPerCU = 0;
+    hipOccupancyMaxActiveBlocksPerMultiprocessor(&blocksPerCU, (const void*)k_mega, 256, 0);
+    if (blocksPerCU < 1) blocksPerCU = 1;
+    int grid = blocksPerCU * 256;
+    if (grid > 1024) grid = 1024;
+
+    void* args[] = { &p };
+    hipLaunchCooperativeKernel((void*)k_mega, dim3(grid), dim3(256), args, 0, stream);
 }
```
